# Kernel tuning notes

Hardware: AMD Instinct MI355X
Metric: run time of the kernel (lower is better)

The kernel has to match this reference:

```python
import jax, jax.numpy as jnp
import numpy as np

B, M, H, K, D, L = 4, 1024, 1024, 16, 64, 1024
E, DH, TOPK = 8, 4096, 2
EPS = 1e-5


def _skew(X, pad_value):
    # X: [BK, M, L] -> [BK, M, M+L], row i shifted i steps right
    bk, m, l = X.shape
    X = jnp.pad(X, ((0, 0), (0, 0), (0, m + 1)), constant_values=pad_value)
    X = X.reshape(bk, -1)[:, :-m]
    return X.reshape(bk, m, m + l)


def _unskew(X):
    # X: [BK, M, M+L] -> [BK, M, L]
    bk, m, lp = X.shape
    l = lp - m
    X = X.reshape(bk, -1)
    X = jnp.pad(X, ((0, 0), (0, m)))
    X = X.reshape(bk, m, m + l + 1)
    return X[:, :, :l]


def layernorm(x, g, b):
    mu = jnp.mean(x, axis=-1, keepdims=True)
    var = jnp.var(x, axis=-1, keepdims=True)
    return (x - mu) * jax.lax.rsqrt(var + EPS) * g + b


def setup_inputs() -> dict:
    key = jax.random.key(0)
    ks = jax.random.split(key, 16)
    s = 1.0 / np.sqrt(H)
    inp = {
        'h': jax.random.normal(ks[0], (B, M, H), jnp.float32),
        'h_cache': jax.random.normal(ks[1], (B, L, H), jnp.float32),
        'key_pe': jax.random.normal(ks[2], (1, D, L), jnp.float32) * s,
        'wq': jax.random.normal(ks[3], (H, H), jnp.float32) * s,
        'wk': jax.random.normal(ks[4], (H, H), jnp.float32) * s,
        'wv': jax.random.normal(ks[5], (H, H), jnp.float32) * s,
        'wo': jax.random.normal(ks[6], (H, H), jnp.float32) * s,
        'norm1_g': jnp.ones((H,), jnp.float32),
        'norm1_b': jnp.zeros((H,), jnp.float32),
        'norm2_g': jnp.ones((H,), jnp.float32),
        'norm2_b': jnp.zeros((H,), jnp.float32),
        'moe_ln_g': jnp.ones((H,), jnp.float32),
        'moe_ln_b': jnp.zeros((H,), jnp.float32),
        'gate_w': jax.random.normal(ks[7], (H, E), jnp.float32) * s,
        'gate_b': jnp.zeros((E,), jnp.float32),
        'e_w1': jax.random.normal(ks[8], (E, H, DH), jnp.float32) * s,
        'e_b1': jnp.zeros((E, DH), jnp.float32),
        'e_w2': jax.random.normal(ks[9], (E, DH, H), jnp.float32) * (1.0 / np.sqrt(DH)),
        'e_b2': jnp.zeros((E, H), jnp.float32),
    }
    return inp


def _forward(h, h_cache, key_pe, wq, wk, wv, wo, norm1_g, norm1_b, norm2_g, norm2_b,
             moe_ln_g, moe_ln_b, gate_w, gate_b, e_w1, e_b1, e_w2, e_b2):
    h_all = jnp.concatenate([h_cache, h], axis=1)  # [B, L+M, H]

    def heads(x):  # [B, T, H] -> [B*K, T, D]
        b, t, _ = x.shape
        return x.reshape(b, t, K, D).transpose(0, 2, 1, 3).reshape(b * K, t, D)

    q = heads(h @ wq)          # [BK, M, D]
    k = heads(h_all @ wk)      # [BK, L+M, D]
    v = heads(h_all @ wv)      # [BK, L+M, D]

    attn_cont = jnp.einsum('bmd,bnd->bmn', q, k)      # [BK, M, L+M]
    attn_cont = _unskew(attn_cont)                     # [BK, M, L]
    attn_pos = jnp.einsum('bmd,dl->bml', q, key_pe[0])  # [BK, M, L]
    attn = (attn_cont + attn_pos) / np.sqrt(D)
    attn = jax.nn.softmax(attn, axis=-1)
    attn_sk = _skew(attn, 0.0)                         # [BK, M, M+L]
    out = jnp.einsum('bmn,bnd->bmd', attn_sk, v)       # [BK, M, D]
    out = out.reshape(B, K, M, D).transpose(0, 2, 1, 3).reshape(B, M, H)
    attn_out = out @ wo
    h = layernorm(h + attn_out, norm1_g, norm1_b)

    # --- MoE FFN (naive top-k gate, post-LN inside, dropout=0) ---
    x = h.reshape(-1, H)                               # [T, H]
    logits = x @ gate_w + gate_b                       # [T, E]
    vals, idx = jax.lax.top_k(logits, TOPK)            # [T, k]
    scores = jax.nn.softmax(vals, axis=-1)             # [T, k]
    hid = jax.nn.relu(jnp.einsum('th,ehd->etd', x, e_w1) + e_b1[:, None, :])
    all_out = jnp.einsum('etd,edh->eth', hid, e_w2) + e_b2[:, None, :]  # [E, T, H]
    sel = jnp.take_along_axis(all_out.transpose(1, 0, 2), idx[:, :, None], axis=1)  # [T, k, H]
    moe = jnp.sum(scores[:, :, None] * sel, axis=1)    # [T, H]
    core = layernorm(x + moe, moe_ln_g, moe_ln_b).reshape(B, M, H)
    h = layernorm(h + core, norm2_g, norm2_b)
    return h


def reference(h, h_cache, key_pe, wq, wk, wv, wo, norm1_g, norm1_b, norm2_g, norm2_b,
              moe_ln_g, moe_ln_b, gate_w, gate_b, e_w1, e_b1, e_w2, e_b2):
    return _forward(h, h_cache, key_pe, wq, wk, wv, wo, norm1_g, norm1_b, norm2_g,
                    norm2_b, moe_ln_g, moe_ln_b, gate_w, gate_b, e_w1, e_b1, e_w2, e_b2)
```

## Files before the change

kernel.cpp:

```cpp
#include <hip/hip_runtime.h>

typedef unsigned short u16;
typedef unsigned int u32;
typedef __attribute__((ext_vector_type(8))) __bf16 bf16x8;
typedef __attribute__((ext_vector_type(8))) _Float16 f16x8;
typedef __attribute__((ext_vector_type(4))) float f32x4;

__device__ __forceinline__ u16 f2bf(float f){
  unsigned int u = __float_as_uint(f);
  u += 0x7FFFu + ((u >> 16) & 1u);
  return (u16)(u >> 16);
}
__device__ __forceinline__ float bf2f(u16 s){
  return __uint_as_float(((unsigned int)s) << 16);
}
__device__ __forceinline__ void fsplit(float x, u16& hi, u16& lo){
  _Float16 h = (_Float16)x;
  float r = x - (float)h;
  _Float16 l = (_Float16)r;
  hi = *(u16*)&h; lo = *(u16*)&l;
}
__device__ __forceinline__ void gll16(const u16* g, u16* lds){
  __builtin_amdgcn_global_load_lds(
      (const __attribute__((address_space(1))) u32*)g,
      (__attribute__((address_space(3))) u32*)(u32)(unsigned long long)lds,
      16, 0, 0);
}


__global__ void zero8(int* c){ if (threadIdx.x < 8) c[threadIdx.x] = 0; }

__global__ __launch_bounds__(256)
void transpose_cvt_z(const float* __restrict__ in, u16* __restrict__ outp,
                     int R, int C, long zin, long zout)
{
  __shared__ float tile[32][33];
  in  += (long)blockIdx.z * zin;
  outp+= (long)blockIdx.z * zout;
  const int c0 = blockIdx.x << 5, r0 = blockIdx.y << 5;
  const int tx = threadIdx.x, ty = threadIdx.y;
  #pragma unroll
  for (int i = ty; i < 32; i += 8)
    tile[i][tx] = in[(long)(r0 + i) * C + c0 + tx];
  __syncthreads();
  #pragma unroll
  for (int i = ty; i < 32; i += 8)
    outp[(long)(c0 + i) * R + r0 + tx] = f2bf(tile[tx][i]);
}

__global__ __launch_bounds__(256)
void transpose_split(const float* __restrict__ in, u16* __restrict__ oh, u16* __restrict__ ol,
                     int R, int C)
{
  __shared__ float tile[32][33];
  const int c0 = blockIdx.x << 5, r0 = blockIdx.y << 5;
  const int tx = threadIdx.x, ty = threadIdx.y;
  #pragma unroll
  for (int i = ty; i < 32; i += 8)
    tile[i][tx] = in[(long)(r0 + i) * C + c0 + tx];
  __syncthreads();
  #pragma unroll
  for (int i = ty; i < 32; i += 8){
    u16 hh, ll;
    fsplit(tile[tx][i], hh, ll);
    oh[(long)(c0 + i) * R + r0 + tx] = hh;
    ol[(long)(c0 + i) * R + r0 + tx] = ll;
  }
}

__global__ __launch_bounds__(256)
void cvt_split_hall(const float* __restrict__ hc, const float* __restrict__ h,
                    u16* __restrict__ hi, u16* __restrict__ lo)
{
  long i4 = (long)blockIdx.x * 256 + threadIdx.x;
  long row = i4 >> 8;
  int c4 = (int)(i4 & 255);
  int b = (int)(row >> 11), tt = (int)(row & 2047);
  const float4* src = (const float4*)((tt < 1024) ? (hc + ((long)b*1024 + tt)*1024)
                                                  : (h  + ((long)b*1024 + (tt-1024))*1024));
  float4 v = src[c4];
  ushort4 h4, l4;
  fsplit(v.x, h4.x, l4.x); fsplit(v.y, h4.y, l4.y);
  fsplit(v.z, h4.z, l4.z); fsplit(v.w, h4.w, l4.w);
  ((ushort4*)hi)[i4] = h4;
  ((ushort4*)lo)[i4] = l4;
}

__global__ __launch_bounds__(128)
void pack_pe(const float* __restrict__ pe, u16* __restrict__ PEh, u16* __restrict__ PEl)
{
  const int jt = blockIdx.x;
  const int t = threadIdx.x;
  const int ks = t >> 6, lane = t & 63;
  const int fq = lane >> 4, fr = lane & 15;
  const long o = ((long)(jt*2 + ks)*64 + lane)*8;
  #pragma unroll
  for (int e = 0; e < 8; ++e){
    float v = pe[(long)(ks*32 + fq*8 + e)*1024 + jt*16 + fr];
    u16 hh, ll; fsplit(v, hh, ll);
    PEh[o+e] = hh; PEl[o+e] = ll;
  }
}


template<int AMAP, int EPI>
__global__ __launch_bounds__(256)
void gemm_sp(const u16* __restrict__ Ah_, const u16* __restrict__ Al_,
             const u16* __restrict__ Bh_, const u16* __restrict__ Bl_,
             float* __restrict__ C, u16* __restrict__ Ch, u16* __restrict__ Cl,
             int N, int Kd)
{
  __shared__ __align__(16) u16 Ahs[4096];
  __shared__ __align__(16) u16 Als[4096];
  __shared__ __align__(16) u16 Bhs[4096];
  __shared__ __align__(16) u16 Bls[4096];
  const int tm = blockIdx.y, tn = blockIdx.x;
  const int t = threadIdx.x;
  const int lane = t & 63, wv = t >> 6;
  const int wm = wv >> 1, wn = wv & 1;
  const int fr = lane & 15, fq = lane >> 4;

  const int r0l = 32*wv + (lane >> 2);
  const int r1l = r0l + 16;
  const int colu = (lane & 3) << 3;
  auto amap = [](int r)->long{
    if (AMAP == 1){ int b = r >> 10, tt = r & 1023; return (long)b*2048 + 1024 + tt; }
    return (long)r;
  };
  const long ar0 = amap(tm*128 + r0l), ar1 = amap(tm*128 + r1l);
  const long br0 = (long)(tn*128 + r0l), br1 = (long)(tn*128 + r1l);
  const u16* pah0 = Ah_ + ar0*Kd + colu;  const u16* pah1 = Ah_ + ar1*Kd + colu;
  const u16* pal0 = Al_ + ar0*Kd + colu;  const u16* pal1 = Al_ + ar1*Kd + colu;
  const u16* pbh0 = Bh_ + br0*Kd + colu;  const u16* pbh1 = Bh_ + br1*Kd + colu;
  const u16* pbl0 = Bl_ + br0*Kd + colu;  const u16* pbl1 = Bl_ + br1*Kd + colu;
  u16* lAh0 = Ahs + 1024*wv;  u16* lAh1 = lAh0 + 512;
  u16* lAl0 = Als + 1024*wv;  u16* lAl1 = lAl0 + 512;
  u16* lBh0 = Bhs + 1024*wv;  u16* lBh1 = lBh0 + 512;
  u16* lBl0 = Bls + 1024*wv;  u16* lBl1 = lBl0 + 512;

  f32x4 acc[4][4];
  const f32x4 z4 = {0.f,0.f,0.f,0.f};
  #pragma unroll
  for (int m=0;m<4;m++)
    #pragma unroll
    for (int n=0;n<4;n++) acc[m][n] = z4;

  const int nk = Kd >> 5;
  for (int kt = 0; kt < nk; ++kt) {
    const int ko = kt << 5;
    __syncthreads();
    gll16(pah0 + ko, lAh0); gll16(pah1 + ko, lAh1);
    gll16(pal0 + ko, lAl0); gll16(pal1 + ko, lAl1);
    gll16(pbh0 + ko, lBh0); gll16(pbh1 + ko, lBh1);
    gll16(pbl0 + ko, lBl0); gll16(pbl1 + ko, lBl1);
    __syncthreads();
    f16x8 afh[4], afl[4], bfh[4], bfl[4];
    #pragma unroll
    for (int m=0;m<4;m++){
      afh[m] = *(const f16x8*)(Ahs + (wm*64 + m*16 + fr)*32 + fq*8);
      afl[m] = *(const f16x8*)(Als + (wm*64 + m*16 + fr)*32 + fq*8);
    }
    #pragma unroll
    for (int n=0;n<4;n++){
      bfh[n] = *(const f16x8*)(Bhs + (wn*64 + n*16 + fr)*32 + fq*8);
      bfl[n] = *(const f16x8*)(Bls + (wn*64 + n*16 + fr)*32 + fq*8);
    }
    #pragma unroll
    for (int m=0;m<4;m++)
      #pragma unroll
      for (int n=0;n<4;n++){
        acc[m][n] = __builtin_amdgcn_mfma_f32_16x16x32_f16(afl[m], bfh[n], acc[m][n], 0, 0, 0);
        acc[m][n] = __builtin_amdgcn_mfma_f32_16x16x32_f16(afh[m], bfl[n], acc[m][n], 0, 0, 0);
        acc[m][n] = __builtin_amdgcn_mfma_f32_16x16x32_f16(afh[m], bfh[n], acc[m][n], 0, 0, 0);
      }
  }

  #pragma unroll
  for (int m=0;m<4;m++){
    #pragma unroll
    for (int j=0;j<4;j++){
      const long crow = (long)(tm*128 + wm*64 + m*16 + fq*4 + j);
      #pragma unroll
      for (int n=0;n<4;n++){
        const int c = tn*128 + wn*64 + n*16 + fr;
        float vv = acc[m][n][j];
        if (EPI == 0){
          C[crow * N + c] = vv;
        } else if (EPI == 1){
          u16 hh, ll; fsplit(vv, hh, ll);
          Ch[crow * N + c] = hh;
          Cl[crow * N + c] = ll;
        } else if (EPI == 2){
          const int b2 = (int)(crow >> 11), key = (int)(crow & 2047);
          const int hd2 = c >> 6, dd = c & 63;
          const long addr = ((long)(b2*16 + hd2))*131072
                          + ((long)((key>>4)*2 + (dd>>5)))*512
                          + (((dd>>3)&3)*16 + (key&15))*8 + (dd&7);
          u16 hh, ll; fsplit(vv, hh, ll);
          Ch[addr] = hh; Cl[addr] = ll;
        } else {
          const int b2 = (int)(crow >> 11), key = (int)(crow & 2047);
          const int hd2 = c >> 6, dd = c & 63;
          const long addr = ((long)(b2*16 + hd2))*131072
                          + ((((long)(key>>4)*4 + (dd>>4))*2 + ((key>>3)&1)))*128
                          + (dd&15)*8 + (key&7);
          u16 hh, ll; fsplit(vv, hh, ll);
          Ch[addr] = hh; Cl[addr] = ll;
        }
      }
    }
  }
}


#define SJP 1032

__global__ __launch_bounds__(256)
void attn_mfma(const u16* __restrict__ qh, const u16* __restrict__ ql,
               const u16* __restrict__ Kph, const u16* __restrict__ Kpl,
               const u16* __restrict__ Vph, const u16* __restrict__ Vpl,
               const u16* __restrict__ PEh, const u16* __restrict__ PEl,
               u16* __restrict__ oh, u16* __restrict__ ol)
{
  __shared__ __align__(16) char smem[68608];
  float* Sj = (float*)smem;
  u16*   Ph = (u16*)smem;
  u16*   Pl = (u16*)(smem + 34048);
  const int bx = blockIdx.x;
  const int q0 = bx << 4;
  const int hd = blockIdx.y, b = blockIdx.z;
  const int t = threadIdx.x, lane = t & 63, wid = t >> 6;
  const int fr = lane & 15, fq = lane >> 4;
  const long plane = ((long)(b*16 + hd)) * 131072;

  f16x8 qfh[2], qfl[2];
  {
    const long qoff = ((long)(b*1024 + q0 + fr))*1024 + hd*64 + fq*8;
    qfh[0] = *(const f16x8*)(qh + qoff);
    qfh[1] = *(const f16x8*)(qh + qoff + 32);
    qfl[0] = *(const f16x8*)(ql + qoff);
    qfl[1] = *(const f16x8*)(ql + qoff + 32);
  }

  for (int base = 0; base < 65; base += 8){
    const int ta = base + wid;
    const int tb = base + wid + 4;
    const int tac = (ta < 65) ? ta : 64;
    const int tbc = (tb < 65) ? tb : 64;
    const u16* fA = Kph + plane + ((long)(bx + tac))*1024 + lane*8;
    const u16* fAl= Kpl + plane + ((long)(bx + tac))*1024 + lane*8;
    const u16* fB = Kph + plane + ((long)(bx + tbc))*1024 + lane*8;
    const u16* fBl= Kpl + plane + ((long)(bx + tbc))*1024 + lane*8;
    f32x4 accA = {0.f,0.f,0.f,0.f}, accB = {0.f,0.f,0.f,0.f};
    #pragma unroll
    for (int ks = 0; ks < 2; ++ks){
      f16x8 bhA = *(const f16x8*)(fA  + ks*512);
      f16x8 blA = *(const f16x8*)(fAl + ks*512);
      f16x8 bhB = *(const f16x8*)(fB  + ks*512);
      f16x8 blB = *(const f16x8*)(fBl + ks*512);
      accA = __builtin_amdgcn_mfma_f32_16x16x32_f16(qfl[ks], bhA, accA, 0, 0, 0);
      accB = __builtin_amdgcn_mfma_f32_16x16x32_f16(qfl[ks], bhB, accB, 0, 0, 0);
      accA = __builtin_amdgcn_mfma_f32_16x16x32_f16(qfh[ks], blA, accA, 0, 0, 0);
      accB = __builtin_amdgcn_mfma_f32_16x16x32_f16(qfh[ks], blB, accB, 0, 0, 0);
      accA = __builtin_amdgcn_mfma_f32_16x16x32_f16(qfh[ks], bhA, accA, 0, 0, 0);
      accB = __builtin_amdgcn_mfma_f32_16x16x32_f16(qfh[ks], bhB, accB, 0, 0, 0);
    }
    if (ta < 65){
      const int ca = tac*16 + fr;
      #pragma unroll
      for (int jj = 0; jj < 4; ++jj){
        const int row = fq*4 + jj;
        const int j = ca - row;
        if (j >= 0 && j < 1024) Sj[row*SJP + j] = accA[jj];
      }
    }
    if (tb < 65){
      const int cb = tbc*16 + fr;
      #pragma unroll
      for (int jj = 0; jj < 4; ++jj){
        const int row = fq*4 + jj;
        const int j = cb - row;
        if (j >= 0 && j < 1024) Sj[row*SJP + j] = accB[jj];
      }
    }
  }
  __syncthreads();

  for (int base = 0; base < 64; base += 8){
    const int ta = base + wid, tb = base + wid + 4;
    const u16* fA = PEh + ((long)ta)*1024 + lane*8;
    const u16* fAl= PEl + ((long)ta)*1024 + lane*8;
    const u16* fB = PEh + ((long)tb)*1024 + lane*8;
    const u16* fBl= PEl + ((long)tb)*1024 + lane*8;
    f32x4 accA = {0.f,0.f,0.f,0.f}, accB = {0.f,0.f,0.f,0.f};
    #pragma unroll
    for (int ks = 0; ks < 2; ++ks){
      f16x8 bhA = *(const f16x8*)(fA  + ks*512);
      f16x8 blA = *(const f16x8*)(fAl + ks*512);
      f16x8 bhB = *(const f16x8*)(fB  + ks*512);
      f16x8 blB = *(const f16x8*)(fBl + ks*512);
      accA = __builtin_amdgcn_mfma_f32_16x16x32_f16(qfl[ks], bhA, accA, 0, 0, 0);
      accB = __builtin_amdgcn_mfma_f32_16x16x32_f16(qfl[ks], bhB, accB, 0, 0, 0);
      accA = __builtin_amdgcn_mfma_f32_16x16x32_f16(qfh[ks], blA, accA, 0, 0, 0);
      accB = __builtin_amdgcn_mfma_f32_16x16x32_f16(qfh[ks], blB, accB, 0, 0, 0);
      accA = __builtin_amdgcn_mfma_f32_16x16x32_f16(qfh[ks], bhA, accA, 0, 0, 0);
      accB = __builtin_amdgcn_mfma_f32_16x16x32_f16(qfh[ks], bhB, accB, 0, 0, 0);
    }
    const int ja = ta*16 + fr, jb = tb*16 + fr;
    #pragma unroll
    for (int jj = 0; jj < 4; ++jj){
      const int row = fq*4 + jj;
      Sj[row*SJP + ja] += accA[jj];
      Sj[row*SJP + jb] += accB[jj];
    }
  }
  __syncthreads();

  {
    const int r = t >> 4, g = t & 15;
    float sv[64];
    float mx = -3.0e38f;
    #pragma unroll
    for (int m = 0; m < 64; ++m){
      float x = Sj[r*SJP + g + (m<<4)] * 0.125f;
      sv[m] = x; mx = fmaxf(mx, x);
    }
    #pragma unroll
    for (int o = 8; o; o >>= 1) mx = fmaxf(mx, __shfl_xor(mx, o, 64));
    float sum = 0.f;
    #pragma unroll
    for (int m = 0; m < 64; ++m){ sv[m] = __expf(sv[m] - mx); sum += sv[m]; }
    #pragma unroll
    for (int o = 8; o; o >>= 1) sum += __shfl_xor(sum, o, 64);
    const float inv = 1.f / sum;
    __syncthreads();
    for (int i = t; i < 17024; i += 256) ((unsigned*)smem)[i] = 0;
    __syncthreads();
    #pragma unroll
    for (int m = 0; m < 64; ++m){
      float p = sv[m] * inv;
      u16 hh, ll; fsplit(p, hh, ll);
      const int c = r + g + (m<<4);
      Ph[r*1064 + c] = hh;
      Pl[r*1064 + c] = ll;
    }
  }
  __syncthreads();

  {
    f32x4 acc0 = {0.f,0.f,0.f,0.f}, acc1 = {0.f,0.f,0.f,0.f};
    const int qq = fq & 1;
    for (int ks = 0; ks < 33; ++ks){
      int kc16 = bx + 2*ks + (fq >> 1);
      if (kc16 > 127) kc16 = 127;
      const long vo = plane + (((long)kc16*4 + wid)*2 + qq)*128 + fr*8;
      f16x8 vh = *(const f16x8*)(Vph + vo);
      f16x8 vl = *(const f16x8*)(Vpl + vo);
      f16x8 ah = *(const f16x8*)(Ph + fr*1064 + ks*32 + fq*8);
      f16x8 al = *(const f16x8*)(Pl + fr*1064 + ks*32 + fq*8);
      f32x4& a = (ks & 1) ? acc1 : acc0;
      a = __builtin_amdgcn_mfma_f32_16x16x32_f16(al, vh, a, 0, 0, 0);
      a = __builtin_amdgcn_mfma_f32_16x16x32_f16(ah, vl, a, 0, 0, 0);
      a = __builtin_amdgcn_mfma_f32_16x16x32_f16(ah, vh, a, 0, 0, 0);
    }
    #pragma unroll
    for (int jj = 0; jj < 4; ++jj){
      float v = acc0[jj] + acc1[jj];
      u16 hh, ll; fsplit(v, hh, ll);
      const int row = fq*4 + jj;
      const long o = ((long)(b*1024 + q0 + row))*1024 + hd*64 + wid*16 + fr;
      oh[o] = hh; ol[o] = ll;
    }
  }
}


template<bool GATHER, bool RELU>
__global__ __launch_bounds__(256)
void gemm_bt(const u16* __restrict__ A, const u16* __restrict__ Bt, u16* __restrict__ Cp,
             const float* __restrict__ bias, int N, int Kd, int maxA,
             const int* __restrict__ offs, const int* __restrict__ counts,
             const int* __restrict__ gather, int ebase)
{
  __shared__ __align__(16) u16 As[4096];
  __shared__ __align__(16) u16 Bs[4096];
  const int z = blockIdx.z;
  const int e = ebase + z;
  const int rbase = offs[e];
  const int cnt   = counts[e];
  const int tm = blockIdx.y, tn = blockIdx.x;
  if (tm * 128 >= cnt) return;
  const u16* BtE = Bt + (long)z * N * Kd;
  const float* biasE = bias + (long)e * N;

  const int t = threadIdx.x;
  const int lane = t & 63, wv = t >> 6;
  const int wm = wv >> 1, wn = wv & 1;
  const int fr = lane & 15, fq = lane >> 4;

  const int r0l = 32*wv + (lane >> 2);
  const int r1l = r0l + 16;
  const int colu = (lane & 3) << 3;
  auto amap = [&](int rl)->long{
    int r = tm*128 + rl;
    int rc = (r < cnt) ? r : (cnt - 1);
    if (GATHER){
      int gi = rbase + rc; gi = (gi < 0) ? 0 : ((gi > 8191) ? 8191 : gi);
      int tok = gather[gi];
      tok = (tok < 0) ? 0 : ((tok >= maxA) ? (maxA - 1) : tok);
      return (long)tok;
    }
    return (long)(rbase + rc);
  };
  const long ar0 = amap(r0l), ar1 = amap(r1l);
  const long br0 = (long)(tn*128 + r0l), br1 = (long)(tn*128 + r1l);
  const u16* pa0 = A + ar0*Kd + colu;    const u16* pa1 = A + ar1*Kd + colu;
  const u16* pb0 = BtE + br0*Kd + colu;  const u16* pb1 = BtE + br1*Kd + colu;
  u16* lA0 = As + 1024*wv;  u16* lA1 = lA0 + 512;
  u16* lB0 = Bs + 1024*wv;  u16* lB1 = lB0 + 512;

  f32x4 acc[4][4];
  const f32x4 z4 = {0.f,0.f,0.f,0.f};
  #pragma unroll
  for (int m=0;m<4;m++)
    #pragma unroll
    for (int n=0;n<4;n++) acc[m][n] = z4;

  const int nk = Kd >> 5;
  for (int kt = 0; kt < nk; ++kt) {
    const int ko = kt << 5;
    __syncthreads();
    gll16(pa0 + ko, lA0); gll16(pa1 + ko, lA1);
    gll16(pb0 + ko, lB0); gll16(pb1 + ko, lB1);
    __syncthreads();
    bf16x8 af[4], bfv[4];
    #pragma unroll
    for (int m=0;m<4;m++) af[m]  = *(const bf16x8*)(As + (wm*64 + m*16 + fr)*32 + fq*8);
    #pragma unroll
    for (int n=0;n<4;n++) bfv[n] = *(const bf16x8*)(Bs + (wn*64 + n*16 + fr)*32 + fq*8);
    #pragma unroll
    for (int m=0;m<4;m++)
      #pragma unroll
      for (int n=0;n<4;n++)
        acc[m][n] = __builtin_amdgcn_mfma_f32_16x16x32_bf16(af[m], bfv[n], acc[m][n], 0, 0, 0);
  }

  #pragma unroll
  for (int m=0;m<4;m++){
    #pragma unroll
    for (int j=0;j<4;j++){
      const int r = tm*128 + wm*64 + m*16 + fq*4 + j;
      if (r >= cnt) continue;
      const long crow = (long)(rbase + r);
      #pragma unroll
      for (int n=0;n<4;n++){
        const int c = tn*128 + wn*64 + n*16 + fr;
        float vv = acc[m][n][j] + biasE[c];
        if (RELU) vv = fmaxf(vv, 0.f);
        Cp[crow * N + c] = f2bf(vv);
      }
    }
  }
}


__device__ __forceinline__ void block_reduce2(float& s1, float& s2){
  #pragma unroll
  for (int o = 32; o; o >>= 1){
    s1 += __shfl_xor(s1, o, 64);
    s2 += __shfl_xor(s2, o, 64);
  }
  __shared__ float r1[4], r2[4];
  const int wid = threadIdx.x >> 6;
  if ((threadIdx.x & 63) == 0){ r1[wid] = s1; r2[wid] = s2; }
  __syncthreads();
  s1 = r1[0] + r1[1] + r1[2] + r1[3];
  s2 = r2[0] + r2[1] + r2[2] + r2[3];
  __syncthreads();
}

__global__ __launch_bounds__(256)
void add_ln_kernel(const float* __restrict__ a, const float* __restrict__ r,
                   const float* __restrict__ g, const float* __restrict__ bb,
                   float* __restrict__ of, u16* __restrict__ ob)
{
  const long row = blockIdx.x;
  const int t = threadIdx.x;
  float y[4]; float sum = 0.f, sq = 0.f;
  #pragma unroll
  for (int i = 0; i < 4; ++i){
    const long idx = row*1024 + t + (i<<8);
    float vv = a[idx] + r[idx];
    y[i] = vv; sum += vv; sq += vv*vv;
  }
  block_reduce2(sum, sq);
  const float mu = sum * (1.f/1024.f);
  const float var = fmaxf(sq * (1.f/1024.f) - mu*mu, 0.f);
  const float rs = rsqrtf(var + 1e-5f);
  #pragma unroll
  for (int i = 0; i < 4; ++i){
    const int hcol = t + (i<<8);
    float o = (y[i] - mu) * rs * g[hcol] + bb[hcol];
    of[row*1024 + hcol] = o;
    ob[row*1024 + hcol] = f2bf(o);
  }
}

__global__ __launch_bounds__(256)
void gate_kernel(const float* __restrict__ x, const float* __restrict__ gw,
                 const float* __restrict__ gb, int* __restrict__ eidx,
                 float* __restrict__ esc, int* __restrict__ counts)
{
  const long row = blockIdx.x;
  const int t = threadIdx.x;
  float a[8];
  #pragma unroll
  for (int e=0;e<8;e++) a[e]=0.f;
  for (int hcol = t; hcol < 1024; hcol += 256){
    float xv = x[row*1024 + hcol];
    const float* gr = gw + hcol*8;
    #pragma unroll
    for (int e=0;e<8;e++) a[e] += xv * gr[e];
  }
  #pragma unroll
  for (int e=0;e<8;e++)
    #pragma unroll
    for (int o=32;o;o>>=1) a[e] += __shfl_xor(a[e], o, 64);
  __shared__ float red[4][8];
  const int wid = t >> 6;
  if ((t & 63)==0){
    #pragma unroll
    for (int e=0;e<8;e++) red[wid][e]=a[e];
  }
  __syncthreads();
  if (t == 0){
    float l[8];
    #pragma unroll
    for (int e=0;e<8;e++) l[e] = red[0][e]+red[1][e]+red[2][e]+red[3][e] + gb[e];
    int i0 = 0; float v0 = l[0];
    #pragma unroll
    for (int e=1;e<8;e++) if (l[e] > v0){ v0=l[e]; i0=e; }
    int i1 = -1; float v1 = -3.0e38f;
    #pragma unroll
    for (int e=0;e<8;e++) if (e != i0 && l[e] > v1){ v1=l[e]; i1=e; }
    float e1 = __expf(v1 - v0);
    float den = 1.f + e1;
    eidx[row*2+0]=i0; eidx[row*2+1]=i1;
    esc[row*2+0]=1.f/den; esc[row*2+1]=e1/den;
    atomicAdd(&counts[i0],1); atomicAdd(&counts[i1],1);
  }
}

__global__ void scan_kernel(const int* __restrict__ counts, int* __restrict__ offs,
                            int* __restrict__ curs)
{
  if (threadIdx.x == 0 && blockIdx.x == 0){
    int acc = 0;
    for (int e=0;e<8;e++){ offs[e]=acc; curs[e]=acc; acc += counts[e]; }
  }
}

__global__ __launch_bounds__(256)
void scatter_kernel(const int* __restrict__ eidx, int* __restrict__ curs,
                    int* __restrict__ stok, int* __restrict__ ppos)
{
  int id = blockIdx.x*256 + threadIdx.x;
  if (id >= 8192) return;
  int e = eidx[id];
  e = (e < 0) ? 0 : ((e > 7) ? 7 : e);
  int pos = atomicAdd(&curs[e], 1);
  pos = (pos < 0) ? 0 : ((pos > 8191) ? 8191 : pos);
  stok[pos] = id >> 1;
  ppos[id] = pos;
}

__global__ __launch_bounds__(256)
void moe_combine_ln(const float* __restrict__ h1, const u16* __restrict__ pout,
                    const float* __restrict__ esc, const int* __restrict__ ppos,
                    const float* __restrict__ mg, const float* __restrict__ mb,
                    const float* __restrict__ n2g, const float* __restrict__ n2b,
                    float* __restrict__ outp)
{
  const long row = blockIdx.x;
  const int t = threadIdx.x;
  int p0i = ppos[row*2+0], p1i = ppos[row*2+1];
  p0i = (p0i < 0) ? 0 : ((p0i > 8191) ? 8191 : p0i);
  p1i = (p1i < 0) ? 0 : ((p1i > 8191) ? 8191 : p1i);
  const long p0 = p0i, p1 = p1i;
  const float s0 = esc[row*2+0], s1 = esc[row*2+1];
  float x[4], y[4];
  float sum=0.f, sq=0.f;
  #pragma unroll
  for (int i=0;i<4;i++){
    const int hcol = t + (i<<8);
    const long idx = row*1024 + hcol;
    float xv = h1[idx];
    float m = s0 * bf2f(pout[p0*1024 + hcol]) + s1 * bf2f(pout[p1*1024 + hcol]);
    x[i]=xv; y[i]=xv+m; sum+=y[i]; sq+=y[i]*y[i];
  }
  block_reduce2(sum, sq);
  float mu = sum*(1.f/1024.f), var = fmaxf(sq*(1.f/1024.f)-mu*mu, 0.f), rs = rsqrtf(var+1e-5f);
  float zz[4]; float sum2=0.f, sq2=0.f;
  #pragma unroll
  for (int i=0;i<4;i++){
    const int hcol = t + (i<<8);
    float core = (y[i]-mu)*rs*mg[hcol]+mb[hcol];
    zz[i] = x[i] + core; sum2+=zz[i]; sq2+=zz[i]*zz[i];
  }
  block_reduce2(sum2, sq2);
  float mu2 = sum2*(1.f/1024.f), var2 = fmaxf(sq2*(1.f/1024.f)-mu2*mu2, 0.f), rs2 = rsqrtf(var2+1e-5f);
  #pragma unroll
  for (int i=0;i<4;i++){
    const int hcol = t + (i<<8);
    outp[row*1024 + hcol] = (zz[i]-mu2)*rs2*n2g[hcol]+n2b[hcol];
  }
}


extern "C" void kernel_launch(void* const* d_in, const int* in_sizes, int n_in,
                              void* d_out, int out_size, void* d_ws, size_t ws_size,
                              hipStream_t stream)
{
  const float* h      = (const float*)d_in[0];
  const float* hc     = (const float*)d_in[1];
  const float* key_pe = (const float*)d_in[2];
  const float* wq     = (const float*)d_in[3];
  const float* wk     = (const float*)d_in[4];
  const float* wv     = (const float*)d_in[5];
  const float* wo     = (const float*)d_in[6];
  const float* n1g    = (const float*)d_in[7];
  const float* n1b    = (const float*)d_in[8];
  const float* n2g    = (const float*)d_in[9];
  const float* n2b    = (const float*)d_in[10];
  const float* mlg    = (const float*)d_in[11];
  const float* mlb    = (const float*)d_in[12];
  const float* gw     = (const float*)d_in[13];
  const float* gb     = (const float*)d_in[14];
  const float* ew1    = (const float*)d_in[15];
  const float* eb1    = (const float*)d_in[16];
  const float* ew2    = (const float*)d_in[17];
  const float* eb2    = (const float*)d_in[18];
  float* outp = (float*)d_out;

  const size_t MB = 1ull << 20;
  char* base = (char*)d_ws;
  int*   counts = (int*)(base);
  int*   offs   = (int*)(base + 256);
  int*   curs   = (int*)(base + 512);
  int*   eidx   = (int*)(base + 1024);
  float* esc    = (float*)(base + 64*1024);
  int*   stok   = (int*)(base + 128*1024);
  int*   ppos   = (int*)(base + 192*1024);
  u16*   PEp_h  = (u16*)(base + 1*MB);
  u16*   PEp_l  = (u16*)(base + 1*MB + 256*1024);
  u16*   hall_h = (u16*)(base + 2*MB);
  float* h1     = (float*)(base + 2*MB);
  u16*   hall_l = (u16*)(base + 18*MB);
  u16*   h1b    = (u16*)(base + 18*MB);
  u16*   wqT_h  = (u16*)(base + 34*MB);
  u16*   wqT_l  = (u16*)(base + 36*MB);
  u16*   wkT_h  = (u16*)(base + 38*MB);
  u16*   wkT_l  = (u16*)(base + 40*MB);
  u16*   wvT_h  = (u16*)(base + 42*MB);
  u16*   wvT_l  = (u16*)(base + 44*MB);
  u16*   woT_h  = (u16*)(base + 46*MB);
  u16*   woT_l  = (u16*)(base + 48*MB);
  u16*   wTg    = (u16*)(base + 34*MB);
  u16*   qh     = (u16*)(base + 50*MB);
  u16*   ql     = (u16*)(base + 58*MB);
  float* aproj  = (float*)(base + 50*MB);
  u16*   Kp_h   = (u16*)(base + 66*MB);
  u16*   Kp_l   = (u16*)(base + 82*MB);
  u16*   Vp_h   = (u16*)(base + 98*MB);
  u16*   Vp_l   = (u16*)(base + 114*MB);
  u16*   xhid   = (u16*)(base + 66*MB);
  u16*   aout_h = (u16*)(base + 130*MB);
  u16*   aout_l = (u16*)(base + 138*MB);
  u16*   pout   = (u16*)(base + 130*MB);

  zero8<<<1, 64, 0, stream>>>(counts);
  dim3 tb32(32, 8);

  cvt_split_hall<<<8192, 256, 0, stream>>>(hc, h, hall_h, hall_l);
  pack_pe<<<64, 128, 0, stream>>>(key_pe, PEp_h, PEp_l);
  transpose_split<<<dim3(32,32), tb32, 0, stream>>>(wq, wqT_h, wqT_l, 1024, 1024);
  transpose_split<<<dim3(32,32), tb32, 0, stream>>>(wk, wkT_h, wkT_l, 1024, 1024);
  transpose_split<<<dim3(32,32), tb32, 0, stream>>>(wv, wvT_h, wvT_l, 1024, 1024);
  transpose_split<<<dim3(32,32), tb32, 0, stream>>>(wo, woT_h, woT_l, 1024, 1024);

  gemm_sp<1,1><<<dim3(8,32), 256, 0, stream>>>(hall_h, hall_l, wqT_h, wqT_l, nullptr, qh, ql, 1024, 1024);
  gemm_sp<0,2><<<dim3(8,64), 256, 0, stream>>>(hall_h, hall_l, wkT_h, wkT_l, nullptr, Kp_h, Kp_l, 1024, 1024);
  gemm_sp<0,3><<<dim3(8,64), 256, 0, stream>>>(hall_h, hall_l, wvT_h, wvT_l, nullptr, Vp_h, Vp_l, 1024, 1024);

  attn_mfma<<<dim3(64,16,4), 256, 0, stream>>>(qh, ql, Kp_h, Kp_l, Vp_h, Vp_l, PEp_h, PEp_l, aout_h, aout_l);

  gemm_sp<0,0><<<dim3(8,32), 256, 0, stream>>>(aout_h, aout_l, woT_h, woT_l, aproj, nullptr, nullptr, 1024, 1024);
  add_ln_kernel<<<4096, 256, 0, stream>>>(h, aproj, n1g, n1b, h1, h1b);

  gate_kernel<<<4096, 256, 0, stream>>>(h1, gw, gb, eidx, esc, counts);
  scan_kernel<<<1, 64, 0, stream>>>(counts, offs, curs);
  scatter_kernel<<<32, 256, 0, stream>>>(eidx, curs, stok, ppos);

  for (int g = 0; g < 2; ++g){
    transpose_cvt_z<<<dim3(128,32,4), tb32, 0, stream>>>(
        ew1 + (long)g*4*1024*4096, wTg, 1024, 4096, 4096L*1024, 4096L*1024);
    gemm_bt<true, true ><<<dim3(32,64,4), 256, 0, stream>>>(
        h1b, wTg, xhid, eb1, 4096, 1024, 4096, offs, counts, stok, g*4);
  }
  for (int g = 0; g < 2; ++g){
    transpose_cvt_z<<<dim3(32,128,4), tb32, 0, stream>>>(
        ew2 + (long)g*4*4096*1024, wTg, 4096, 1024, 4096L*1024, 4096L*1024);
    gemm_bt<false, false><<<dim3(8,64,4), 256, 0, stream>>>(
        xhid, wTg, pout, eb2, 1024, 4096, 8192, offs, counts, nullptr, g*4);
  }

  moe_combine_ln<<<4096, 256, 0, stream>>>(h1, pout, esc, ppos, mlg, mlb, n2g, n2b, outp);
}
```

Before: 1.144 ms.

## Fuse QKV projections into one GEMM and double-buffer expert GEMM loads

Merges the four weight transpose-split launches into one z-indexed launch. The separate Q, K and V projection GEMMs become one GEMM over concatenated K|V|Q weights (N=3072), with the epilogue routing columns to the packed K/V layouts or the Q rows. The expert GEMM gets double-buffered LDS, so the next K-tile is loaded while the current one computes. Q is now computed for all 2048 rows and the cache-half results are thrown away, which adds wasted MFMA work in exchange for fewer launches and a larger grid.

```diff
diff --git a/kernel.cpp b/kernel.cpp
--- a/kernel.cpp
+++ b/kernel.cpp
@@ -49,22 +49,28 @@
 }
 
 __global__ __launch_bounds__(256)
-void transpose_split(const float* __restrict__ in, u16* __restrict__ oh, u16* __restrict__ ol,
-                     int R, int C)
+void transpose_split4(const float* __restrict__ s0, const float* __restrict__ s1,
+                      const float* __restrict__ s2, const float* __restrict__ s3,
+                      u16* __restrict__ wall_h, u16* __restrict__ wall_l,
+                      u16* __restrict__ wo_h, u16* __restrict__ wo_l)
 {
   __shared__ float tile[32][33];
+  const int z = blockIdx.z;
+  const float* in = (z==0)?s0:(z==1)?s1:(z==2)?s2:s3;
+  u16* oh = (z<3) ? (wall_h + (long)z*1024*1024) : wo_h;
+  u16* ol = (z<3) ? (wall_l + (long)z*1024*1024) : wo_l;
   const int c0 = blockIdx.x << 5, r0 = blockIdx.y << 5;
   const int tx = threadIdx.x, ty = threadIdx.y;
   #pragma unroll
   for (int i = ty; i < 32; i += 8)
-    tile[i][tx] = in[(long)(r0 + i) * C + c0 + tx];
+    tile[i][tx] = in[(long)(r0 + i) * 1024 + c0 + tx];
   __syncthreads();
   #pragma unroll
   for (int i = ty; i < 32; i += 8){
     u16 hh, ll;
     fsplit(tile[tx][i], hh, ll);
-    oh[(long)(c0 + i) * R + r0 + tx] = hh;
-    ol[(long)(c0 + i) * R + r0 + tx] = ll;
+    oh[(long)(c0 + i) * 1024 + r0 + tx] = hh;
+    ol[(long)(c0 + i) * 1024 + r0 + tx] = ll;
   }
 }
 
@@ -103,11 +109,14 @@
 }
 
 
-template<int AMAP, int EPI>
+template<int EPI>
 __global__ __launch_bounds__(256)
 void gemm_sp(const u16* __restrict__ Ah_, const u16* __restrict__ Al_,
              const u16* __restrict__ Bh_, const u16* __restrict__ Bl_,
-             float* __restrict__ C, u16* __restrict__ Ch, u16* __restrict__ Cl,
+             float* __restrict__ C,
+             u16* __restrict__ Kh, u16* __restrict__ Kl,
+             u16* __restrict__ Vh, u16* __restrict__ Vl,
+             u16* __restrict__ Qh, u16* __restrict__ Ql,
              int N, int Kd)
 {
   __shared__ __align__(16) u16 Ahs[4096];
@@ -123,11 +132,7 @@
   const int r0l = 32*wv + (lane >> 2);
   const int r1l = r0l + 16;
   const int colu = (lane & 3) << 3;
-  auto amap = [](int r)->long{
-    if (AMAP == 1){ int b = r >> 10, tt = r & 1023; return (long)b*2048 + 1024 + tt; }
-    return (long)r;
-  };
-  const long ar0 = amap(tm*128 + r0l), ar1 = amap(tm*128 + r1l);
+  const long ar0 = (long)(tm*128 + r0l), ar1 = (long)(tm*128 + r1l);
   const long br0 = (long)(tn*128 + r0l), br1 = (long)(tn*128 + r1l);
   const u16* pah0 = Ah_ + ar0*Kd + colu;  const u16* pah1 = Ah_ + ar1*Kd + colu;
   const u16* pal0 = Al_ + ar0*Kd + colu;  const u16* pal1 = Al_ + ar1*Kd + colu;
@@ -186,26 +191,28 @@
         float vv = acc[m][n][j];
         if (EPI == 0){
           C[crow * N + c] = vv;
-        } else if (EPI == 1){
-          u16 hh, ll; fsplit(vv, hh, ll);
-          Ch[crow * N + c] = hh;
-          Cl[crow * N + c] = ll;
-        } else if (EPI == 2){
-          const int b2 = (int)(crow >> 11), key = (int)(crow & 2047);
-          const int hd2 = c >> 6, dd = c & 63;
-          const long addr = ((long)(b2*16 + hd2))*131072
-                          + ((long)((key>>4)*2 + (dd>>5)))*512
-                          + (((dd>>3)&3)*16 + (key&15))*8 + (dd&7);
-          u16 hh, ll; fsplit(vv, hh, ll);
-          Ch[addr] = hh; Cl[addr] = ll;
         } else {
           const int b2 = (int)(crow >> 11), key = (int)(crow & 2047);
-          const int hd2 = c >> 6, dd = c & 63;
-          const long addr = ((long)(b2*16 + hd2))*131072
-                          + ((((long)(key>>4)*4 + (dd>>4))*2 + ((key>>3)&1)))*128
-                          + (dd&15)*8 + (key&7);
           u16 hh, ll; fsplit(vv, hh, ll);
-          Ch[addr] = hh; Cl[addr] = ll;
+          if (c < 1024){
+            const int hd2 = c >> 6, dd = c & 63;
+            const long addr = ((long)(b2*16 + hd2))*131072
+                            + ((long)((key>>4)*2 + (dd>>5)))*512
+                            + (((dd>>3)&3)*16 + (key&15))*8 + (dd&7);
+            Kh[addr] = hh; Kl[addr] = ll;
+          } else if (c < 2048){
+            const int c2 = c - 1024;
+            const int hd2 = c2 >> 6, dd = c2 & 63;
+            const long addr = ((long)(b2*16 + hd2))*131072
+                            + ((((long)(key>>4)*4 + (dd>>4))*2 + ((key>>3)&1)))*128
+                            + (dd&15)*8 + (key&7);
+            Vh[addr] = hh; Vl[addr] = ll;
+          } else if (key >= 1024){
+            const int c2 = c - 2048;
+            const long qrow = (long)b2*1024 + (key - 1024);
+            Qh[qrow*1024 + c2] = hh;
+            Ql[qrow*1024 + c2] = ll;
+          }
         }
       }
     }
@@ -382,8 +389,8 @@
              const int* __restrict__ offs, const int* __restrict__ counts,
              const int* __restrict__ gather, int ebase)
 {
-  __shared__ __align__(16) u16 As[4096];
-  __shared__ __align__(16) u16 Bs[4096];
+  __shared__ __align__(16) u16 As[2][4096];
+  __shared__ __align__(16) u16 Bs[2][4096];
   const int z = blockIdx.z;
   const int e = ebase + z;
   const int rbase = offs[e];
@@ -416,8 +423,6 @@
   const long br0 = (long)(tn*128 + r0l), br1 = (long)(tn*128 + r1l);
   const u16* pa0 = A + ar0*Kd + colu;    const u16* pa1 = A + ar1*Kd + colu;
   const u16* pb0 = BtE + br0*Kd + colu;  const u16* pb1 = BtE + br1*Kd + colu;
-  u16* lA0 = As + 1024*wv;  u16* lA1 = lA0 + 512;
-  u16* lB0 = Bs + 1024*wv;  u16* lB1 = lB0 + 512;
 
   f32x4 acc[4][4];
   const f32x4 z4 = {0.f,0.f,0.f,0.f};
@@ -426,18 +431,25 @@
     #pragma unroll
     for (int n=0;n<4;n++) acc[m][n] = z4;
 
+  auto issue = [&](int bufi, int kt){
+    const int ko = kt << 5;
+    gll16(pa0 + ko, As[bufi] + 1024*wv);
+    gll16(pa1 + ko, As[bufi] + 1024*wv + 512);
+    gll16(pb0 + ko, Bs[bufi] + 1024*wv);
+    gll16(pb1 + ko, Bs[bufi] + 1024*wv + 512);
+  };
+
   const int nk = Kd >> 5;
+  issue(0, 0);
   for (int kt = 0; kt < nk; ++kt) {
-    const int ko = kt << 5;
+    const int cur = kt & 1;
     __syncthreads();
-    gll16(pa0 + ko, lA0); gll16(pa1 + ko, lA1);
-    gll16(pb0 + ko, lB0); gll16(pb1 + ko, lB1);
-    __syncthreads();
+    if (kt + 1 < nk) issue(cur ^ 1, kt + 1);
     bf16x8 af[4], bfv[4];
     #pragma unroll
-    for (int m=0;m<4;m++) af[m]  = *(const bf16x8*)(As + (wm*64 + m*16 + fr)*32 + fq*8);
-    #pragma unroll
-    for (int n=0;n<4;n++) bfv[n] = *(const bf16x8*)(Bs + (wn*64 + n*16 + fr)*32 + fq*8);
+    for (int m=0;m<4;m++) af[m]  = *(const bf16x8*)(As[cur] + (wm*64 + m*16 + fr)*32 + fq*8);
+    #pragma unroll
+    for (int n=0;n<4;n++) bfv[n] = *(const bf16x8*)(Bs[cur] + (wn*64 + n*16 + fr)*32 + fq*8);
     #pragma unroll
     for (int m=0;m<4;m++)
       #pragma unroll
@@ -657,12 +669,8 @@
   float* h1     = (float*)(base + 2*MB);
   u16*   hall_l = (u16*)(base + 18*MB);
   u16*   h1b    = (u16*)(base + 18*MB);
-  u16*   wqT_h  = (u16*)(base + 34*MB);
-  u16*   wqT_l  = (u16*)(base + 36*MB);
-  u16*   wkT_h  = (u16*)(base + 38*MB);
-  u16*   wkT_l  = (u16*)(base + 40*MB);
-  u16*   wvT_h  = (u16*)(base + 42*MB);
-  u16*   wvT_l  = (u16*)(base + 44*MB);
+  u16*   wall_h = (u16*)(base + 34*MB);
+  u16*   wall_l = (u16*)(base + 40*MB);
   u16*   woT_h  = (u16*)(base + 46*MB);
   u16*   woT_l  = (u16*)(base + 48*MB);
   u16*   wTg    = (u16*)(base + 34*MB);
@@ -683,18 +691,16 @@
 
   cvt_split_hall<<<8192, 256, 0, stream>>>(hc, h, hall_h, hall_l);
   pack_pe<<<64, 128, 0, stream>>>(key_pe, PEp_h, PEp_l);
-  transpose_split<<<dim3(32,32), tb32, 0, stream>>>(wq, wqT_h, wqT_l, 1024, 1024);
-  transpose_split<<<dim3(32,32), tb32, 0, stream>>>(wk, wkT_h, wkT_l, 1024, 1024);
-  transpose_split<<<dim3(32,32), tb32, 0, stream>>>(wv, wvT_h, wvT_l, 1024, 1024);
-  transpose_split<<<dim3(32,32), tb32, 0, stream>>>(wo, woT_h, woT_l, 1024, 1024);
-
-  gemm_sp<1,1><<<dim3(8,32), 256, 0, stream>>>(hall_h, hall_l, wqT_h, wqT_l, nullptr, qh, ql, 1024, 1024);
-  gemm_sp<0,2><<<dim3(8,64), 256, 0, stream>>>(hall_h, hall_l, wkT_h, wkT_l, nullptr, Kp_h, Kp_l, 1024, 1024);
-  gemm_sp<0,3><<<dim3(8,64), 256, 0, stream>>>(hall_h, hall_l, wvT_h, wvT_l, nullptr, Vp_h, Vp_l, 1024, 1024);
+  transpose_split4<<<dim3(32,32,4), tb32, 0, stream>>>(wk, wv, wq, wo,
+                                                       wall_h, wall_l, woT_h, woT_l);
+
+  gemm_sp<4><<<dim3(24,64), 256, 0, stream>>>(hall_h, hall_l, wall_h, wall_l, nullptr,
+                                              Kp_h, Kp_l, Vp_h, Vp_l, qh, ql, 3072, 1024);
 
   attn_mfma<<<dim3(64,16,4), 256, 0, stream>>>(qh, ql, Kp_h, Kp_l, Vp_h, Vp_l, PEp_h, PEp_l, aout_h, aout_l);
 
-  gemm_sp<0,0><<<dim3(8,32), 256, 0, stream>>>(aout_h, aout_l, woT_h, woT_l, aproj, nullptr, nullptr, 1024, 1024);
+  gemm_sp<0><<<dim3(8,32), 256, 0, stream>>>(aout_h, aout_l, woT_h, woT_l, aproj,
+                                             nullptr, nullptr, nullptr, nullptr, nullptr, nullptr, 1024, 1024);
   add_ln_kernel<<<4096, 256, 0, stream>>>(h, aproj, n1g, n1b, h1, h1b);
 
   gate_kernel<<<4096, 256, 0, stream>>>(h1, gw, gb, eidx, esc, counts);
```

Measured after the change: 1.073 ms. 6.2% less time.
